# Performance work log

Hardware: AMD Instinct MI355X
Metric: run time of the kernel (lower is better)

Reference implementation:

```python
import jax, jax.numpy as jnp
import numpy as np

N_SRC = 50000
N_DST = 50000
IN_FEATS = 256
OUT_FEATS = 32
NUM_HEADS = 4
N_EDGES = 800000


def setup_inputs() -> dict:
    key = jax.random.key(0)
    ks = jax.random.split(key, 7)
    h_src = jax.random.normal(ks[0], (N_SRC, IN_FEATS), dtype=jnp.float32)
    h_dst = jax.random.normal(ks[1], (N_DST, IN_FEATS), dtype=jnp.float32)
    # xavier-normal-ish scaling for the shared fc weight
    W = jax.random.normal(ks[2], (IN_FEATS, NUM_HEADS * OUT_FEATS), dtype=jnp.float32) * (
        jnp.sqrt(2.0) * jnp.sqrt(2.0 / (IN_FEATS + NUM_HEADS * OUT_FEATS))
    )
    attn_l = jax.random.normal(ks[3], (NUM_HEADS, OUT_FEATS), dtype=jnp.float32) * 0.1
    attn_r = jax.random.normal(ks[4], (NUM_HEADS, OUT_FEATS), dtype=jnp.float32) * 0.1
    src_idx = jax.random.randint(ks[5], (N_EDGES,), 0, N_SRC, dtype=jnp.int32)
    dst_idx = jax.random.randint(ks[6], (N_EDGES,), 0, N_DST, dtype=jnp.int32)
    return {"h_src": h_src, "h_dst": h_dst, "W": W, "attn_l": attn_l,
            "attn_r": attn_r, "src_idx": src_idx, "dst_idx": dst_idx}


def reference(h_src, h_dst, W, attn_l, attn_r, src_idx, dst_idx):
    H, F = NUM_HEADS, OUT_FEATS
    # shared linear projection (no bias), reshape to [N, H, F]
    ft_src = (h_src @ W).reshape(-1, H, F)            # [N_src, H, F]
    ft_dst = (h_dst @ W).reshape(-1, H, F)            # [N_dst, H, F]
    # per-node attention logits, [N, H]
    el = jnp.einsum('nhf,hf->nh', ft_src, attn_l)
    er = jnp.einsum('nhf,hf->nh', ft_dst, attn_r)
    # u_add_v gather over edges, LeakyReLU(0.2) -> [E, H]
    e = jax.nn.leaky_relu(el[src_idx] + er[dst_idx], negative_slope=0.2)
    # edge softmax over incoming edges of each destination node
    smax = jax.ops.segment_max(e, dst_idx, num_segments=N_DST)   # [N_dst, H]
    e_exp = jnp.exp(e - smax[dst_idx])                           # [E, H]
    ssum = jax.ops.segment_sum(e_exp, dst_idx, num_segments=N_DST)
    a = e_exp / ssum[dst_idx]                                    # [E, H]
    # u_mul_e + scatter-sum aggregation -> [N_dst, H, F]
    msg = ft_src[src_idx] * a[:, :, None]
    rst = jax.ops.segment_sum(msg, dst_idx, num_segments=N_DST)
    return rst
```

## Files before the change

kernel.cpp:

```cpp
#include <hip/hip_runtime.h>

#define IN_FEATS 256
#define OUT_FEATS 32
#define NUM_HEADS 4
#define NHF 128

#define NCH 256
#define PRE 13

typedef __attribute__((ext_vector_type(8))) short short8;
typedef __attribute__((ext_vector_type(4))) float f32x4;

__device__ inline unsigned short f2bf(float f) {
    unsigned int u = __builtin_bit_cast(unsigned int, f);
    u = (u + 0x7fff + ((u >> 16) & 1)) >> 16;
    return (unsigned short)u;
}
__device__ inline float bfhi2f(unsigned int packed_hi) {
    return __builtin_bit_cast(float, packed_hi);
}

__global__ __launch_bounds__(256) void prep_hist(const float* __restrict__ W,
                                                 const float* __restrict__ attn_r,
                                                 const int* __restrict__ dst,
                                                 float* __restrict__ v,
                                                 unsigned short* __restrict__ Wt,
                                                 int* __restrict__ bcnt,
                                                 int E) {
    const int t = threadIdx.x;
    const int b = blockIdx.x;
    if (b < 128) {
        Wt[b * 256 + t] = f2bf(W[(size_t)t * NHF + b]);
    } else if (b == 128) {
        for (int p = t; p < IN_FEATS * NUM_HEADS; p += 256) {
            int k = p >> 2, h = p & 3;
            const float* wr = W + (size_t)k * NHF + h * OUT_FEATS;
            const float* ar = attn_r + h * OUT_FEATS;
            float s = 0.f;
            #pragma unroll
            for (int f = 0; f < OUT_FEATS; ++f) s += wr[f] * ar[f];
            v[p] = s;
        }
    } else {
        __shared__ int cnt[256];
        const int hb = b - 129;
        const int chunk = (E + NCH - 1) / NCH;
        const int e0 = hb * chunk;
        const int e1 = min(e0 + chunk, E);
        cnt[t] = 0;
        __syncthreads();
        for (int e = e0 + t; e < e1; e += 256)
            atomicAdd(&cnt[dst[e] >> 8], 1);
        __syncthreads();
        int c = cnt[t];
        if (c) atomicAdd(&bcnt[t], c);
    }
}

#define BSTRIDE 136
__global__ __launch_bounds__(256) void bin_gemm(const int* __restrict__ src,
                                                const int* __restrict__ dst,
                                                const int* __restrict__ bcnt,
                                                int* __restrict__ bcursor,
                                                unsigned int* __restrict__ pairs,
                                                int* __restrict__ bbase,
                                                int E,
                                                const float* __restrict__ A,
                                                const unsigned short* __restrict__ Wt,
                                                const float* __restrict__ attn_l,
                                                unsigned short* __restrict__ ft16,
                                                float* __restrict__ el, int M,
                                                int ngb) {
    __shared__ unsigned short WtL[128 * 256];

    if ((int)blockIdx.x >= ngb) {
        int* sc    = (int*)WtL;
        int* basel = (int*)WtL + 256;
        int* cnt   = (int*)WtL + 512;
        const int t = threadIdx.x;
        const int b = blockIdx.x - ngb;
        const int chunk = (E + NCH - 1) / NCH;
        const int e0 = b * chunk;
        const int e1 = min(e0 + chunk, E);

        int dreg[PRE], sreg[PRE];
        #pragma unroll
        for (int i = 0; i < PRE; ++i) {
            const int e = e0 + t + i * 256;
            const bool ok = e < e1;
            dreg[i] = ok ? dst[e] : 0;
            sreg[i] = ok ? src[e] : 0;
        }

        cnt[t] = 0;
        __syncthreads();
        #pragma unroll
        for (int i = 0; i < PRE; ++i) {
            const int e = e0 + t + i * 256;
            if (e < e1) atomicAdd(&cnt[dreg[i] >> 8], 1);
        }
        for (int e = e0 + t + PRE * 256; e < e1; e += 256)
            atomicAdd(&cnt[dst[e] >> 8], 1);
        __syncthreads();
        const int myc = cnt[t];

        const int bv = bcnt[t];
        sc[t] = bv;
        __syncthreads();
        #pragma unroll
        for (int d = 1; d < 256; d <<= 1) {
            int x = (t >= d) ? sc[t - d] : 0;
            __syncthreads();
            sc[t] += x;
            __syncthreads();
        }
        const int bb_t = sc[t] - bv;
        if (b == 0) {
            bbase[t] = bb_t;
            if (t == 255) bbase[256] = sc[255];
        }

        basel[t] = myc ? (bb_t + atomicAdd(&bcursor[t], myc)) : 0;
        cnt[t] = 0;
        __syncthreads();

        #pragma unroll
        for (int i = 0; i < PRE; ++i) {
            const int e = e0 + t + i * 256;
            if (e < e1) {
                const int d = dreg[i];
                const int bk = d >> 8;
                const int o = atomicAdd(&cnt[bk], 1);
                pairs[basel[bk] + o] = (unsigned int)sreg[i] | ((unsigned int)(d & 255) << 16);
            }
        }
        for (int e = e0 + t + PRE * 256; e < e1; e += 256) {
            const int d = dst[e];
            const int bk = d >> 8;
            const int o = atomicAdd(&cnt[bk], 1);
            pairs[basel[bk] + o] = (unsigned int)src[e] | ((unsigned int)(d & 255) << 16);
        }
        return;
    }

    const int gb   = blockIdx.x;
    const int wave = threadIdx.x >> 6;
    const int lane = threadIdx.x & 63;
    const int quad = lane >> 4;
    const int mc   = lane & 15;
    const int row_base = gb * 64 + wave * 16;

    for (int i = threadIdx.x; i < 4096; i += 256) {
        const int n = i >> 5, c = i & 31;
        const int cs = (c + n) & 31;
        *(uint4*)(WtL + n * 256 + cs * 8) = *(const uint4*)(Wt + n * 256 + c * 8);
    }

    float al[8];
    #pragma unroll
    for (int t = 0; t < 8; ++t) al[t] = attn_l[(t >> 1) * 32 + (t & 1) * 16 + mc];

    const int rowA = min(row_base + mc, M - 1);
    const float* arow = A + (size_t)rowA * IN_FEATS;

    float4 a[8][2];
    #pragma unroll
    for (int kk = 0; kk < 8; ++kk) {
        a[kk][0] = *(const float4*)(arow + kk * 32 + quad * 8);
        a[kk][1] = *(const float4*)(arow + kk * 32 + quad * 8 + 4);
    }

    f32x4 acc[8];
    #pragma unroll
    for (int t = 0; t < 8; ++t) acc[t] = (f32x4){0.f, 0.f, 0.f, 0.f};

    __syncthreads();

    #pragma unroll
    for (int kk = 0; kk < 8; ++kk) {
        short8 af;
        af[0] = (short)f2bf(a[kk][0].x); af[1] = (short)f2bf(a[kk][0].y);
        af[2] = (short)f2bf(a[kk][0].z); af[3] = (short)f2bf(a[kk][0].w);
        af[4] = (short)f2bf(a[kk][1].x); af[5] = (short)f2bf(a[kk][1].y);
        af[6] = (short)f2bf(a[kk][1].z); af[7] = (short)f2bf(a[kk][1].w);
        #pragma unroll
        for (int t = 0; t < 8; ++t) {
            const int n = t * 16 + mc;
            const int c = ((kk << 2) + quad + n) & 31;
            const short8 bf = *(const short8*)(WtL + n * 256 + c * 8);
            acc[t] = __builtin_amdgcn_mfma_f32_16x16x32_bf16(af, bf, acc[t], 0, 0, 0);
        }
    }

    float elp[4][4];
    #pragma unroll
    for (int v = 0; v < 4; ++v)
        #pragma unroll
        for (int h = 0; h < 4; ++h) elp[v][h] = 0.f;
    #pragma unroll
    for (int v = 0; v < 4; ++v)
        #pragma unroll
        for (int t = 0; t < 8; ++t) elp[v][t >> 1] += acc[t][v] * al[t];
    #pragma unroll
    for (int v = 0; v < 4; ++v)
        #pragma unroll
        for (int h = 0; h < 4; ++h) {
            #pragma unroll
            for (int d = 1; d < 16; d <<= 1)
                elp[v][h] += __shfl_xor(elp[v][h], d, 64);
        }

    #pragma unroll
    for (int v = 0; v < 4; ++v) {
        const int rg = row_base + quad * 4 + v;
        if (rg < M && mc < 4) {
            float ev = (mc == 0) ? elp[v][0] : (mc == 1) ? elp[v][1]
                     : (mc == 2) ? elp[v][2] : elp[v][3];
            el[(size_t)rg * 4 + mc] = ev;
        }
    }

    __syncthreads();
    #pragma unroll
    for (int v = 0; v < 4; ++v) {
        const int lr = wave * 16 + quad * 4 + v;
        #pragma unroll
        for (int t = 0; t < 8; ++t)
            WtL[lr * BSTRIDE + t * 16 + mc] = f2bf(acc[t][v]);
    }
    __syncthreads();
    const int rows_in_blk = min(64, M - gb * 64);
    for (int i = threadIdx.x; i < 64 * 16; i += 256) {
        const int lr = i >> 4, seg = i & 15;
        if (lr < rows_in_blk)
            *(uint4*)(ft16 + (size_t)(gb * 64 + lr) * NHF + seg * 8) =
                *(const uint4*)(WtL + lr * BSTRIDE + seg * 8);
    }
}

__global__ __launch_bounds__(256) void er_fine(const float* __restrict__ hdst,
                                               const float* __restrict__ v,
                                               float* __restrict__ er, int M,
                                               const unsigned int* __restrict__ pairs,
                                               const int* __restrict__ bbase,
                                               int* __restrict__ off,
                                               unsigned short* __restrict__ csr16,
                                               int nb, int n_dst, int E) {
    __shared__ int cnt[256];
    __shared__ int cur[256];

    if (blockIdx.x < (unsigned)nb) {
        const int t = threadIdx.x;
        const int b = blockIdx.x;
        const int p0 = bbase[b], p1 = bbase[b + 1];
        cnt[t] = 0;
        __syncthreads();
        for (int p = p0 + t; p < p1; p += 256)
            atomicAdd(&cnt[pairs[p] >> 16], 1);
        __syncthreads();
        int vv = cnt[t];
        cur[t] = vv;
        __syncthreads();
        #pragma unroll
        for (int d = 1; d < 256; d <<= 1) {
            int x = (t >= d) ? cur[t - d] : 0;
            __syncthreads();
            cur[t] += x;
            __syncthreads();
        }
        int ex = cur[t] - vv;
        int node = b * 256 + t;
        if (node < n_dst) off[node] = p0 + ex;
        if (b == 0 && t == 0) off[n_dst] = E;
        __syncthreads();
        cur[t] = ex;
        __syncthreads();
        for (int p = p0 + t; p < p1; p += 256) {
            unsigned int pr = pairs[p];
            int o = atomicAdd(&cur[pr >> 16], 1);
            csr16[p0 + o] = (unsigned short)(pr & 0xffffu);
        }
        return;
    }

    int wid  = ((blockIdx.x - nb) * 256 + threadIdx.x) >> 6;
    int lane = threadIdx.x & 63;
    if (wid >= M) return;
    const float4 x = *(const float4*)(hdst + (size_t)wid * IN_FEATS + lane * 4);
    const float4* vp = (const float4*)(v + (size_t)lane * 16);
    float4 v0 = vp[0], v1 = vp[1], v2 = vp[2], v3 = vp[3];
    float a0 = x.x * v0.x + x.y * v1.x + x.z * v2.x + x.w * v3.x;
    float a1 = x.x * v0.y + x.y * v1.y + x.z * v2.y + x.w * v3.y;
    float a2 = x.x * v0.z + x.y * v1.z + x.z * v2.z + x.w * v3.z;
    float a3 = x.x * v0.w + x.y * v1.w + x.z * v2.w + x.w * v3.w;
    #pragma unroll
    for (int m = 32; m >= 1; m >>= 1) {
        a0 += __shfl_xor(a0, m, 64);
        a1 += __shfl_xor(a1, m, 64);
        a2 += __shfl_xor(a2, m, 64);
        a3 += __shfl_xor(a3, m, 64);
    }
    if (lane == 0) *(float4*)(er + (size_t)wid * 4) = make_float4(a0, a1, a2, a3);
}

__global__ __launch_bounds__(256) void agg_pull(const int* __restrict__ off,
                                                const unsigned short* __restrict__ csr16,
                                                const float* __restrict__ el,
                                                const float* __restrict__ er,
                                                const uint2* __restrict__ ftp,
                                                float* __restrict__ out, int n_dst) {
    const int wid  = (blockIdx.x * blockDim.x + threadIdx.x) >> 6;
    const int lane = threadIdx.x & 63;
    const int half = lane >> 5;
    const int hl   = lane & 31;
    const int node = wid * 2 + half;
    const bool valid = node < n_dst;
    const int nc = valid ? node : 0;
    const int h  = hl >> 3;
    const float er_h = er[nc * 4 + h];
    const int start = off[nc];
    const int end   = valid ? off[nc + 1] : start;
    const int deg   = end - start;
    const int last  = max(end - 1, 0);

    const int sl = (int)csr16[min(start + hl, last)];

    const int mdeg  = max(deg, __shfl_xor(deg, 32, 64));
    const int iters = (min(mdeg, 32) + 7) >> 3;

    float a0 = 0.f, a1 = 0.f, a2 = 0.f, a3 = 0.f, sw = 0.f;

    float e[8]; uint2 q[8];
    #pragma unroll
    for (int j = 0; j < 8; ++j) {
        const int s = __shfl(sl, j, 32);
        e[j] = el[s * 4 + h];
        q[j] = ftp[s * 32 + hl];
    }

    for (int i = 0; i < iters; ++i) {
        float f[8]; uint2 r[8];
        const int jn = (i + 1) << 3;
        #pragma unroll
        for (int j = 0; j < 8; ++j) {
            const int s = __shfl(sl, min(jn + j, 31), 32);
            f[j] = el[s * 4 + h];
            r[j] = ftp[s * 32 + hl];
        }

        const int kb = start + (i << 3);
        #pragma unroll
        for (int j = 0; j < 8; ++j) {
            float x = e[j] + er_h;
            x = fmaxf(x, 0.2f * x);
            const float w = (kb + j < end) ? __expf(x) : 0.f;
            sw += w;
            a0 = fmaf(bfhi2f(q[j].x << 16),          w, a0);
            a1 = fmaf(bfhi2f(q[j].x & 0xffff0000u),  w, a1);
            a2 = fmaf(bfhi2f(q[j].y << 16),          w, a2);
            a3 = fmaf(bfhi2f(q[j].y & 0xffff0000u),  w, a3);
        }

        #pragma unroll
        for (int j = 0; j < 8; ++j) { e[j] = f[j]; q[j] = r[j]; }
    }

    for (int k = start + 32; k < end; ++k) {
        const int s = (int)csr16[k];
        float x = el[s * 4 + h] + er_h;
        x = fmaxf(x, 0.2f * x);
        const float w = __expf(x);
        const uint2 qq = ftp[s * 32 + hl];
        sw += w;
        a0 = fmaf(bfhi2f(qq.x << 16),         w, a0);
        a1 = fmaf(bfhi2f(qq.x & 0xffff0000u), w, a1);
        a2 = fmaf(bfhi2f(qq.y << 16),         w, a2);
        a3 = fmaf(bfhi2f(qq.y & 0xffff0000u), w, a3);
    }

    if (valid) {
        const float inv = (deg > 0) ? 1.f / sw : 0.f;
        float4 r;
        r.x = a0 * inv; r.y = a1 * inv; r.z = a2 * inv; r.w = a3 * inv;
        *(float4*)(out + (size_t)node * NHF + hl * 4) = r;
    }
}

extern "C" void kernel_launch(void* const* d_in, const int* in_sizes, int n_in,
                              void* d_out, int out_size, void* d_ws, size_t ws_size,
                              hipStream_t stream) {
    const float* h_src  = (const float*)d_in[0];
    const float* h_dst  = (const float*)d_in[1];
    const float* W      = (const float*)d_in[2];
    const float* attn_l = (const float*)d_in[3];
    const float* attn_r = (const float*)d_in[4];
    const int* src_idx  = (const int*)d_in[5];
    const int* dst_idx  = (const int*)d_in[6];

    const int n_src = in_sizes[0] / IN_FEATS;
    const int n_dst = in_sizes[1] / IN_FEATS;
    const int E     = in_sizes[5];

    const int nb = (n_dst + 255) >> 8;

    char* ws = (char*)d_ws;
    size_t o = 0;
    float* v       = (float*)(ws + o); o += 4096;
    float* el      = (float*)(ws + o); o += (size_t)n_src * 4 * sizeof(float);
    float* er      = (float*)(ws + o); o += (size_t)n_dst * 4 * sizeof(float);
    int*   off     = (int*)(ws + o);   o += ((size_t)n_dst + 16) * sizeof(int);
    int*   bcnt    = (int*)(ws + o);   o += 256 * sizeof(int);
    int*   bcursor = (int*)(ws + o);   o += 256 * sizeof(int);
    int*   bbase   = (int*)(ws + o);   o += 260 * sizeof(int);
    unsigned short* Wt = (unsigned short*)(ws + o); o += (size_t)NHF * IN_FEATS * sizeof(unsigned short);
    unsigned short* csr16 = (unsigned short*)(ws + o); o += (((size_t)E * 2 + 15) & ~15ull);
    unsigned int* pairs = (unsigned int*)(ws + o); o += (size_t)E * sizeof(unsigned int);
    unsigned short* ft16 = (unsigned short*)(ws + o); o += (size_t)n_src * NHF * sizeof(unsigned short);

    float* out = (float*)d_out;

    const int ngb = (n_src + 63) / 64;

    (void)hipMemsetAsync(bcnt, 0, 512 * sizeof(int), stream);

    prep_hist<<<129 + NCH, 256, 0, stream>>>(W, attn_r, dst_idx, v, Wt, bcnt, E);
    bin_gemm<<<ngb + NCH, 256, 0, stream>>>(src_idx, dst_idx, bcnt, bcursor,
                                            pairs, bbase, E,
                                            h_src, Wt, attn_l, ft16, el, n_src, ngb);
    {
        const int er_blocks = (n_dst * 64 + 255) / 256;
        er_fine<<<nb + er_blocks, 256, 0, stream>>>(h_dst, v, er, n_dst, pairs,
                                                    bbase, off, csr16, nb, n_dst, E);
    }
    {
        const int nwave = (n_dst + 1) >> 1;
        agg_pull<<<(nwave + 3) / 4, 256, 0, stream>>>(off, csr16, el, er,
                                                      (const uint2*)ft16, out, n_dst);
    }
}
```

Measured before the change: 215.9 us.

## Move er computation into bin_gemm launch, split fine CSR build into own kernel

The per-destination er dot-product blocks move from the er_fine launch into the bin_gemm launch as extra trailing blocks. The CSR fine-binning pass becomes its own small kernel with only nb blocks. The goal is to overlap the bandwidth-bound h_dst read with the GEMM and binning work and to shorten the launch that sits on the critical path. The cost is that er blocks now share a launch with blocks that reserve 64KB of LDS, which can limit how many blocks are resident at once.

```diff
diff --git a/kernel.cpp b/kernel.cpp
--- a/kernel.cpp
+++ b/kernel.cpp
@@ -58,20 +58,45 @@
 }
 
 #define BSTRIDE 136
-__global__ __launch_bounds__(256) void bin_gemm(const int* __restrict__ src,
-                                                const int* __restrict__ dst,
-                                                const int* __restrict__ bcnt,
-                                                int* __restrict__ bcursor,
-                                                unsigned int* __restrict__ pairs,
-                                                int* __restrict__ bbase,
-                                                int E,
-                                                const float* __restrict__ A,
-                                                const unsigned short* __restrict__ Wt,
-                                                const float* __restrict__ attn_l,
-                                                unsigned short* __restrict__ ft16,
-                                                float* __restrict__ el, int M,
-                                                int ngb) {
+__global__ __launch_bounds__(256) void bin_gemm_er(const int* __restrict__ src,
+                                                   const int* __restrict__ dst,
+                                                   const int* __restrict__ bcnt,
+                                                   int* __restrict__ bcursor,
+                                                   unsigned int* __restrict__ pairs,
+                                                   int* __restrict__ bbase,
+                                                   int E,
+                                                   const float* __restrict__ A,
+                                                   const unsigned short* __restrict__ Wt,
+                                                   const float* __restrict__ attn_l,
+                                                   unsigned short* __restrict__ ft16,
+                                                   float* __restrict__ el, int M,
+                                                   const float* __restrict__ hdst,
+                                                   const float* __restrict__ v,
+                                                   float* __restrict__ er, int n_dst,
+                                                   int ngb) {
     __shared__ unsigned short WtL[128 * 256];
+
+    if ((int)blockIdx.x >= ngb + NCH) {
+        int wid  = ((blockIdx.x - ngb - NCH) * 256 + threadIdx.x) >> 6;
+        int lane = threadIdx.x & 63;
+        if (wid >= n_dst) return;
+        const float4 x = *(const float4*)(hdst + (size_t)wid * IN_FEATS + lane * 4);
+        const float4* vp = (const float4*)(v + (size_t)lane * 16);
+        float4 v0 = vp[0], v1 = vp[1], v2 = vp[2], v3 = vp[3];
+        float a0 = x.x * v0.x + x.y * v1.x + x.z * v2.x + x.w * v3.x;
+        float a1 = x.x * v0.y + x.y * v1.y + x.z * v2.y + x.w * v3.y;
+        float a2 = x.x * v0.z + x.y * v1.z + x.z * v2.z + x.w * v3.z;
+        float a3 = x.x * v0.w + x.y * v1.w + x.z * v2.w + x.w * v3.w;
+        #pragma unroll
+        for (int m = 32; m >= 1; m >>= 1) {
+            a0 += __shfl_xor(a0, m, 64);
+            a1 += __shfl_xor(a1, m, 64);
+            a2 += __shfl_xor(a2, m, 64);
+            a3 += __shfl_xor(a3, m, 64);
+        }
+        if (lane == 0) *(float4*)(er + (size_t)wid * 4) = make_float4(a0, a1, a2, a3);
+        return;
+    }
 
     if ((int)blockIdx.x >= ngb) {
         int* sc    = (int*)WtL;
@@ -194,39 +219,39 @@
 
     float elp[4][4];
     #pragma unroll
-    for (int v = 0; v < 4; ++v)
-        #pragma unroll
-        for (int h = 0; h < 4; ++h) elp[v][h] = 0.f;
-    #pragma unroll
-    for (int v = 0; v < 4; ++v)
-        #pragma unroll
-        for (int t = 0; t < 8; ++t) elp[v][t >> 1] += acc[t][v] * al[t];
-    #pragma unroll
-    for (int v = 0; v < 4; ++v)
+    for (int v2 = 0; v2 < 4; ++v2)
+        #pragma unroll
+        for (int h = 0; h < 4; ++h) elp[v2][h] = 0.f;
+    #pragma unroll
+    for (int v2 = 0; v2 < 4; ++v2)
+        #pragma unroll
+        for (int t = 0; t < 8; ++t) elp[v2][t >> 1] += acc[t][v2] * al[t];
+    #pragma unroll
+    for (int v2 = 0; v2 < 4; ++v2)
         #pragma unroll
         for (int h = 0; h < 4; ++h) {
             #pragma unroll
             for (int d = 1; d < 16; d <<= 1)
-                elp[v][h] += __shfl_xor(elp[v][h], d, 64);
-        }
-
-    #pragma unroll
-    for (int v = 0; v < 4; ++v) {
-        const int rg = row_base + quad * 4 + v;
+                elp[v2][h] += __shfl_xor(elp[v2][h], d, 64);
+        }
+
+    #pragma unroll
+    for (int v2 = 0; v2 < 4; ++v2) {
+        const int rg = row_base + quad * 4 + v2;
         if (rg < M && mc < 4) {
-            float ev = (mc == 0) ? elp[v][0] : (mc == 1) ? elp[v][1]
-                     : (mc == 2) ? elp[v][2] : elp[v][3];
+            float ev = (mc == 0) ? elp[v2][0] : (mc == 1) ? elp[v2][1]
+                     : (mc == 2) ? elp[v2][2] : elp[v2][3];
             el[(size_t)rg * 4 + mc] = ev;
         }
     }
 
     __syncthreads();
     #pragma unroll
-    for (int v = 0; v < 4; ++v) {
-        const int lr = wave * 16 + quad * 4 + v;
+    for (int v2 = 0; v2 < 4; ++v2) {
+        const int lr = wave * 16 + quad * 4 + v2;
         #pragma unroll
         for (int t = 0; t < 8; ++t)
-            WtL[lr * BSTRIDE + t * 16 + mc] = f2bf(acc[t][v]);
+            WtL[lr * BSTRIDE + t * 16 + mc] = f2bf(acc[t][v2]);
     }
     __syncthreads();
     const int rows_in_blk = min(64, M - gb * 64);
@@ -238,69 +263,43 @@
     }
 }
 
-__global__ __launch_bounds__(256) void er_fine(const float* __restrict__ hdst,
-                                               const float* __restrict__ v,
-                                               float* __restrict__ er, int M,
-                                               const unsigned int* __restrict__ pairs,
-                                               const int* __restrict__ bbase,
-                                               int* __restrict__ off,
-                                               unsigned short* __restrict__ csr16,
-                                               int nb, int n_dst, int E) {
+__global__ __launch_bounds__(256) void fine(const unsigned int* __restrict__ pairs,
+                                            const int* __restrict__ bbase,
+                                            int* __restrict__ off,
+                                            unsigned short* __restrict__ csr16,
+                                            int n_dst, int E) {
     __shared__ int cnt[256];
     __shared__ int cur[256];
-
-    if (blockIdx.x < (unsigned)nb) {
-        const int t = threadIdx.x;
-        const int b = blockIdx.x;
-        const int p0 = bbase[b], p1 = bbase[b + 1];
-        cnt[t] = 0;
-        __syncthreads();
-        for (int p = p0 + t; p < p1; p += 256)
-            atomicAdd(&cnt[pairs[p] >> 16], 1);
-        __syncthreads();
-        int vv = cnt[t];
-        cur[t] = vv;
-        __syncthreads();
-        #pragma unroll
-        for (int d = 1; d < 256; d <<= 1) {
-            int x = (t >= d) ? cur[t - d] : 0;
-            __syncthreads();
-            cur[t] += x;
-            __syncthreads();
-        }
-        int ex = cur[t] - vv;
-        int node = b * 256 + t;
-        if (node < n_dst) off[node] = p0 + ex;
-        if (b == 0 && t == 0) off[n_dst] = E;
-        __syncthreads();
-        cur[t] = ex;
-        __syncthreads();
-        for (int p = p0 + t; p < p1; p += 256) {
-            unsigned int pr = pairs[p];
-            int o = atomicAdd(&cur[pr >> 16], 1);
-            csr16[p0 + o] = (unsigned short)(pr & 0xffffu);
-        }
-        return;
-    }
-
-    int wid  = ((blockIdx.x - nb) * 256 + threadIdx.x) >> 6;
-    int lane = threadIdx.x & 63;
-    if (wid >= M) return;
-    const float4 x = *(const float4*)(hdst + (size_t)wid * IN_FEATS + lane * 4);
-    const float4* vp = (const float4*)(v + (size_t)lane * 16);
-    float4 v0 = vp[0], v1 = vp[1], v2 = vp[2], v3 = vp[3];
-    float a0 = x.x * v0.x + x.y * v1.x + x.z * v2.x + x.w * v3.x;
-    float a1 = x.x * v0.y + x.y * v1.y + x.z * v2.y + x.w * v3.y;
-    float a2 = x.x * v0.z + x.y * v1.z + x.z * v2.z + x.w * v3.z;
-    float a3 = x.x * v0.w + x.y * v1.w + x.z * v2.w + x.w * v3.w;
-    #pragma unroll
-    for (int m = 32; m >= 1; m >>= 1) {
-        a0 += __shfl_xor(a0, m, 64);
-        a1 += __shfl_xor(a1, m, 64);
-        a2 += __shfl_xor(a2, m, 64);
-        a3 += __shfl_xor(a3, m, 64);
-    }
-    if (lane == 0) *(float4*)(er + (size_t)wid * 4) = make_float4(a0, a1, a2, a3);
+    const int t = threadIdx.x;
+    const int b = blockIdx.x;
+    const int p0 = bbase[b], p1 = bbase[b + 1];
+    cnt[t] = 0;
+    __syncthreads();
+    for (int p = p0 + t; p < p1; p += 256)
+        atomicAdd(&cnt[pairs[p] >> 16], 1);
+    __syncthreads();
+    int vv = cnt[t];
+    cur[t] = vv;
+    __syncthreads();
+    #pragma unroll
+    for (int d = 1; d < 256; d <<= 1) {
+        int x = (t >= d) ? cur[t - d] : 0;
+        __syncthreads();
+        cur[t] += x;
+        __syncthreads();
+    }
+    int ex = cur[t] - vv;
+    int node = b * 256 + t;
+    if (node < n_dst) off[node] = p0 + ex;
+    if (b == 0 && t == 0) off[n_dst] = E;
+    __syncthreads();
+    cur[t] = ex;
+    __syncthreads();
+    for (int p = p0 + t; p < p1; p += 256) {
+        unsigned int pr = pairs[p];
+        int o = atomicAdd(&cur[pr >> 16], 1);
+        csr16[p0 + o] = (unsigned short)(pr & 0xffffu);
+    }
 }
 
 __global__ __launch_bounds__(256) void agg_pull(const int* __restrict__ off,
@@ -420,18 +419,16 @@
     float* out = (float*)d_out;
 
     const int ngb = (n_src + 63) / 64;
+    const int ner = (n_dst * 64 + 255) / 256;
 
     (void)hipMemsetAsync(bcnt, 0, 512 * sizeof(int), stream);
 
     prep_hist<<<129 + NCH, 256, 0, stream>>>(W, attn_r, dst_idx, v, Wt, bcnt, E);
-    bin_gemm<<<ngb + NCH, 256, 0, stream>>>(src_idx, dst_idx, bcnt, bcursor,
-                                            pairs, bbase, E,
-                                            h_src, Wt, attn_l, ft16, el, n_src, ngb);
-    {
-        const int er_blocks = (n_dst * 64 + 255) / 256;
-        er_fine<<<nb + er_blocks, 256, 0, stream>>>(h_dst, v, er, n_dst, pairs,
-                                                    bbase, off, csr16, nb, n_dst, E);
-    }
+    bin_gemm_er<<<ngb + NCH + ner, 256, 0, stream>>>(src_idx, dst_idx, bcnt, bcursor,
+                                                     pairs, bbase, E,
+                                                     h_src, Wt, attn_l, ft16, el, n_src,
+                                                     h_dst, v, er, n_dst, ngb);
+    fine<<<nb, 256, 0, stream>>>(pairs, bbase, off, csr16, n_dst, E);
     {
         const int nwave = (n_dst + 1) >> 1;
         agg_pull<<<(nwave + 3) / 4, 256, 0, stream>>>(off, csr16, el, er,
```

New measurement: 245.7 us. 1.14x slower.
